# Kernel optimization log

Hardware: AMD Instinct MI355X
Metric: run time of the kernel (lower is better)

The kernel has to match this reference:

```python
import jax, jax.numpy as jnp
import numpy as np

B, M, N = 64, 100, 100
LAMBDA_COORD = 1.0
LAMBDA_CONF = 1.0
EPS = 1e-12


def _hungarian(cost):
    """O(n^3) Hungarian algorithm (potentials / e-maxx variant) on a square
    numpy cost matrix. Returns row_to_col assignment (length n)."""
    n = cost.shape[0]
    u = np.zeros(n + 1)
    v = np.zeros(n + 1)
    p = np.zeros(n + 1, dtype=np.int64)   # p[j] = row matched to column j
    way = np.zeros(n + 1, dtype=np.int64)
    for i in range(1, n + 1):
        p[0] = i
        j0 = 0
        minv = np.full(n + 1, np.inf)
        used = np.zeros(n + 1, dtype=bool)
        while True:
            used[j0] = True
            i0 = p[j0]
            js = np.nonzero(~used)[0]
            js = js[js > 0]
            cur = cost[i0 - 1, js - 1] - u[i0] - v[js]
            upd = cur < minv[js]
            minv[js] = np.where(upd, cur, minv[js])
            way[js] = np.where(upd, j0, way[js])
            j1 = js[np.argmin(minv[js])]
            delta = minv[j1]
            uj = np.nonzero(used)[0]
            u[p[uj]] += delta
            v[uj] -= delta
            minv[js] -= delta
            j0 = j1
            if p[j0] == 0:
                break
        while j0:
            j1 = way[j0]
            p[j0] = p[j1]
            j0 = j1
    row_to_col = np.full(n, -1, dtype=np.int64)
    for j in range(1, n + 1):
        row_to_col[p[j] - 1] = j - 1
    return row_to_col


def _match(pred_xy, target_xy, target_conf):
    """Host-side matching (mirrors the original's CPU round trip).
    Returns padded rows [B,P], cols [B,P] (cols index into the ORIGINAL target
    axis) and cnt [B] = number of matched pairs (min(M, K_valid))."""
    Bb, Mm, _ = pred_xy.shape
    Nn = target_xy.shape[1]
    P = min(Mm, Nn)
    rows = np.zeros((Bb, P), np.int64)
    cols = np.zeros((Bb, P), np.int64)
    cnt = np.zeros(Bb, np.int64)
    for b in range(Bb):
        valid = np.nonzero(target_conf[b] > 0.5)[0]
        K = valid.size
        if K == 0:
            continue
        tgt = target_xy[b, valid]                       # [K,2]
        cost = np.linalg.norm(pred_xy[b][:, None, :] - tgt[None, :, :], axis=-1)  # [M,K]
        n = max(Mm, K)
        sq = np.zeros((n, n))                           # zero-pad to square
        sq[:Mm, :K] = cost
        r2c = _hungarian(sq)
        k = 0
        for r in range(Mm):
            c = r2c[r]
            if 0 <= c < K:
                rows[b, k] = r
                cols[b, k] = valid[c]
                k += 1
        cnt[b] = k
    return rows, cols, cnt


def _loss(pred, target, rows, cols, cnt):
    Bb, P = rows.shape
    bidx = jnp.arange(Bb)[:, None]
    mp = pred[bidx, rows]                                # [B,P,3] matched preds
    mt = target[bidx, cols]                              # [B,P,3] matched tgts
    mask = (jnp.arange(P)[None, :] < cnt[:, None]).astype(pred.dtype)
    denom = jnp.maximum(cnt, 1).astype(pred.dtype)
    # per-batch F.mse_loss: mean over cnt*2 coord elements
    se = (((mp[..., :2] - mt[..., :2]) ** 2).sum(-1) * mask).sum(-1)
    loss_coord = jnp.where(cnt > 0, se / (2.0 * denom), 0.0).sum()
    # per-batch F.binary_cross_entropy: mean over cnt elements
    pconf = jnp.clip(mp[..., 2], EPS, 1.0 - EPS)
    tconf = mt[..., 2]
    bce = -(tconf * jnp.log(pconf) + (1.0 - tconf) * jnp.log1p(-pconf))
    loss_conf = jnp.where(cnt > 0, (bce * mask).sum(-1) / denom, 0.0).sum()
    return (LAMBDA_COORD * loss_coord + LAMBDA_CONF * loss_conf) / Bb


def setup_inputs() -> dict:
    key = jax.random.key(0)
    k1, k2 = jax.random.split(key)
    pred = jax.random.uniform(k1, (B, M, 3), dtype=jnp.float32)
    target = jax.random.uniform(k2, (B, N, 3), dtype=jnp.float32)
    return {"pred": pred, "target": target}


def reference(pred, target):
    pred_np = np.asarray(pred)
    tgt_np = np.asarray(target)
    rows, cols, cnt = _match(pred_np[..., :2], tgt_np[..., :2], tgt_np[..., 2])
    rows = jnp.asarray(rows)
    cols = jnp.asarray(cols)
    cnt = jnp.asarray(cnt)
    return _loss(pred, target, rows, cols, cnt)
```

## Files before the change

### kernel.cpp

```cpp
#include <hip/hip_runtime.h>
#include <math.h>

#define BATCH 64
#define MM 100
#define NN 100
#define ST 101
#define BIGCLAIM 0x7fffffff


__device__ __forceinline__ int readlane_i(int v, int lane) {
    return __builtin_amdgcn_readlane(v, lane);
}
__device__ __forceinline__ float readlane_f(float v, int lane) {
    return __int_as_float(__builtin_amdgcn_readlane(__float_as_int(v), lane));
}

template<int CTRL>
__device__ __forceinline__ float dpp_min_f32(float x) {
    int p = __builtin_amdgcn_update_dpp(__float_as_int(x), __float_as_int(x),
                                        CTRL, 0xF, 0xF, false);
    return fminf(x, __int_as_float(p));
}
__device__ __forceinline__ float wave_min_f32(float x) {
    x = dpp_min_f32<0xB1>(x);
    x = dpp_min_f32<0x4E>(x);
    x = dpp_min_f32<0x141>(x);
    x = dpp_min_f32<0x140>(x);
    x = dpp_min_f32<0x142>(x);
    x = dpp_min_f32<0x143>(x);
    return readlane_f(x, 63);
}


__global__ __launch_bounds__(128) void hungarian_loss_kernel(
        const float* __restrict__ pred, const float* __restrict__ target,
        double* __restrict__ ws) {
    const int b    = blockIdx.x;
    const int tid  = threadIdx.x;
    const int lane = tid & 63;
    const int wave = tid >> 6;
    const float* P = pred + b * MM * 3;
    const float* T = target + b * NN * 3;

    __shared__ float px[MM], py[MM], pc[MM];
    __shared__ float tvx[NN], tvy[NN], tvc[NN];
    __shared__ float Tc[NN * ST];
    __shared__ int   rmini[NN];
    __shared__ int   claimArr[MM + 1];
    __shared__ int   Ksh;

    float pxA = P[3*lane], pyA = P[3*lane+1];
    float pxB = 0.f, pyB = 0.f;
    const bool colBvalid = (lane + 64 < MM);
    if (colBvalid) { pxB = P[3*(lane+64)]; pyB = P[3*(lane+64)+1]; }

    if (wave == 0) {
        px[lane] = pxA; py[lane] = pyA; pc[lane] = P[3*lane+2];
        if (colBvalid) { px[lane+64]=pxB; py[lane+64]=pyB; pc[lane+64]=P[3*(lane+64)+2]; }
        float cxA=0.f, cyA=0.f, ccA=0.f, cxB=0.f, cyB=0.f, ccB=0.f;
        bool vA_=false, vB_=false;
        { cxA=T[3*lane]; cyA=T[3*lane+1]; ccA=T[3*lane+2]; vA_ = ccA > 0.5f; }
        if (lane + 64 < NN) {
            cxB=T[3*(lane+64)]; cyB=T[3*(lane+64)+1]; ccB=T[3*(lane+64)+2];
            vB_ = ccB > 0.5f;
        }
        unsigned long long mAv = __ballot(vA_);
        unsigned long long mBv = __ballot(vB_);
        int nA_ = __popcll(mAv);
        int K0  = nA_ + __popcll(mBv);
        unsigned long long below = (1ull << lane) - 1ull;
        if (vA_) { int q = __popcll(mAv & below);       tvx[q]=cxA; tvy[q]=cyA; tvc[q]=ccA; }
        if (vB_) { int q = nA_ + __popcll(mBv & below); tvx[q]=cxB; tvy[q]=cyB; tvc[q]=ccB; }
        if (lane == 0) Ksh = K0;
        claimArr[lane] = BIGCLAIM;
        if (lane + 64 <= MM) claimArr[lane + 64] = BIGCLAIM;
    }
    __syncthreads();
    const int K = Ksh;
    if (K == 0) { if (tid == 0) ws[b] = 0.0; return; }

    float txA = (lane < K)      ? tvx[lane]      : 0.f;
    float tyA = (lane < K)      ? tvy[lane]      : 0.f;
    float txB = (lane + 64 < K) ? tvx[lane + 64] : 0.f;
    float tyB = (lane + 64 < K) ? tvy[lane + 64] : 0.f;

    for (int c = wave; c < K; c += 2) {
        float tx = (c < 64) ? readlane_f(txA, c) : readlane_f(txB, c - 64);
        float ty = (c < 64) ? readlane_f(tyA, c) : readlane_f(tyB, c - 64);
        float dxA = __fsub_rn(pxA, tx), dyA = __fsub_rn(pyA, ty);
        float cA = __fsqrt_rn(__fadd_rn(__fmul_rn(dxA,dxA), __fmul_rn(dyA,dyA)));
        Tc[c*ST + lane] = cA;
        float cB = 1e30f;
        if (colBvalid) {
            float dxB = __fsub_rn(pxB, tx), dyB = __fsub_rn(pyB, ty);
            cB = __fsqrt_rn(__fadd_rn(__fmul_rn(dxB,dxB), __fmul_rn(dyB,dyB)));
            Tc[c*ST + lane + 64] = cB;
        }
        float m = wave_min_f32(fminf(cA, cB));
        unsigned long long eA = __ballot(cA == m);
        unsigned long long eB = __ballot(cB == m);
        int argc = eA ? ((int)__ffsll(eA) - 1) : ((int)__ffsll(eB) - 1 + 64);
        if (lane == 0) rmini[c] = argc;
    }
    __syncthreads();
    if (wave == 1) return;

    const float INF32 = __builtin_inff();
    const int jA = lane;
    const int jB = lane + 64;
    const bool validB = (jB <= MM);
    const int idxA = (jA >= 1) ? (jA - 1) : 0;
    const int idxB = validB ? (jB - 1) : (MM - 1);

    int rA = lane + 1, rB = lane + 65;
    int argA = 0, argB = 0;
    if (lane < K)      { argA = rmini[lane] + 1;      atomicMin(&claimArr[argA], rA); }
    if (lane + 64 < K) { argB = rmini[lane + 64] + 1; atomicMin(&claimArr[argB], rB); }
    __threadfence_block();
    int pA = 0, pB = 0;
    if (jA >= 1) { int c0 = claimArr[jA]; pA = (c0 != BIGCLAIM) ? c0 : 0; }
    if (validB)  { int c0 = claimArr[jB]; pB = (c0 != BIGCLAIM) ? c0 : 0; }
    bool freeA = (lane < K)      && (claimArr[argA] != rA);
    bool freeB = (lane + 64 < K) && (claimArr[argB] != rB);
    unsigned long long fA = __ballot(freeA);
    unsigned long long fB = __ballot(freeB);

    float vvA = 0.f, vvB = 0.f;

    unsigned long long dijA = 0ull, dijB = 0ull;
    for (int sweep = 0; sweep < 2; ++sweep) {
        unsigned long long curA = fA, curB = fB;
        fA = 0ull; fB = 0ull;
        while (curA | curB) {
            int r;
            if (curA) { r = (int)__ffsll(curA);      curA &= curA - 1; }
            else      { r = (int)__ffsll(curB) + 64; curB &= curB - 1; }

            float cA = Tc[(r-1)*ST + idxA];
            float cB = Tc[(r-1)*ST + idxB];
            float rcA = (jA >= 1) ? (cA - vvA) : INF32;
            float rcB = validB ? (cB - vvB) : INF32;
            float m1 = wave_min_f32(fminf(rcA, rcB));
            unsigned long long eA = __ballot(rcA == m1);
            unsigned long long eB = __ballot(rcB == m1);
            int j1 = eA ? ((int)__ffsll(eA) - 1) : ((int)__ffsll(eB) - 1 + 64);

            float rcA2 = (jA == j1) ? INF32 : rcA;
            float rcB2 = (jB == j1) ? INF32 : rcB;
            float m2 = wave_min_f32(fminf(rcA2, rcB2));

            int holder = (j1 < 64) ? readlane_i(pA, j1) : readlane_i(pB, j1 & 63);

            if (m1 < m2) {
                float dv = m2 - m1;
                if (jA == j1) { vvA -= dv; pA = r; }
                if (validB && jB == j1) { vvB -= dv; pB = r; }
                if (holder != 0) {
                    if (sweep == 0) {
                        if (holder <= 64) fA |= 1ull << (holder - 1);
                        else              fB |= 1ull << (holder - 65);
                    } else {
                        if (holder <= 64) dijA |= 1ull << (holder - 1);
                        else              dijB |= 1ull << (holder - 65);
                    }
                }
            } else {
                if (holder == 0) {
                    if (jA == j1) pA = r;
                    if (validB && jB == j1) pB = r;
                } else {
                    unsigned long long e2A = __ballot(rcA2 == m2);
                    unsigned long long e2B = __ballot(rcB2 == m2);
                    int j2 = e2A ? ((int)__ffsll(e2A) - 1)
                                 : ((int)__ffsll(e2B) - 1 + 64);
                    int h2 = (j2 < 64) ? readlane_i(pA, j2)
                                       : readlane_i(pB, j2 & 63);
                    if (h2 == 0) {
                        if (jA == j2) pA = r;
                        if (validB && jB == j2) pB = r;
                    } else {
                        if (sweep == 0) {
                            if (r <= 64) fA |= 1ull << (r - 1);
                            else         fB |= 1ull << (r - 65);
                        } else {
                            if (r <= 64) dijA |= 1ull << (r - 1);
                            else         dijB |= 1ull << (r - 65);
                        }
                    }
                }
            }
        }
    }

    while (dijA | dijB) {
        int r;
        if (dijA) { r = (int)__ffsll(dijA);      dijA &= dijA - 1; }
        else      { r = (int)__ffsll(dijB) + 64; dijB &= dijB - 1; }

        float minvA = INF32, minvB = INF32;
        int wayA = 0, wayB = 0;
        bool usedA = (lane == 0), usedB = false;
        float dpopA = 0.f, dpopB = 0.f;
        if (lane == 0) pA = r;
        int j0 = 0, jfree = -1;
        float dstar = 0.f;

        float cA_f = Tc[(r-1)*ST + idxA];
        float cB_f = Tc[(r-1)*ST + idxB];
        float S = 0.f;

        for (int it = 0; it <= MM; ++it) {
            float candA = INF32, candB = INF32;
            if (jA >= 1 && !usedA) {
                float t = (cA_f - vvA) + S;
                if (t < minvA) { minvA = t; wayA = j0; }
                candA = minvA;
            }
            if (validB && !usedB) {
                float t = (cB_f - vvB) + S;
                if (t < minvB) { minvB = t; wayB = j0; }
                candB = minvB;
            }

            float delta = wave_min_f32(fminf(candA, candB));
            unsigned long long eA = __ballot(candA == delta);
            unsigned long long eB = __ballot(candB == delta);
            int j1 = eA ? ((int)__ffsll(eA) - 1) : ((int)__ffsll(eB) - 1 + 64);

            if (jA == j1) { usedA = true; dpopA = delta; }
            if (jB == j1) { usedB = true; dpopB = delta; }

            int pa = readlane_i(pA, j1 & 63);
            int pb = readlane_i(pB, j1 & 63);
            int pj1 = (j1 < 64) ? pa : pb;
            if (pj1 == 0) { jfree = j1; dstar = delta; break; }

            float nxA = Tc[(pj1-1)*ST + idxA];
            float nxB = Tc[(pj1-1)*ST + idxB];
            float cjm = (j1 < 64) ? readlane_f(nxA, j1) : readlane_f(nxB, j1 & 63);
            float vjm = (j1 < 64) ? readlane_f(vvA, j1) : readlane_f(vvB, j1 & 63);
            S = (delta - cjm) + vjm;
            cA_f = nxA; cB_f = nxB;
            j0 = j1;
        }

        if (usedA && jA >= 1) vvA += dpopA - dstar;
        if (usedB)            vvB += dpopB - dstar;

        int jc = jfree;
        for (int s = 0; s <= MM && jc > 0; ++s) {
            int wa = readlane_i(wayA, jc & 63);
            int wb = readlane_i(wayB, jc & 63);
            int w  = (jc < 64) ? wa : wb;
            int pa = readlane_i(pA, w & 63);
            int pb = readlane_i(pB, w & 63);
            int pw = (w < 64) ? pa : pb;
            if (jA == jc) pA = pw;
            if (jB == jc) pB = pw;
            jc = w;
        }
    }

    double se = 0.0, bce = 0.0;
    if (jA >= 1 && pA > 0) {
        int rr = jA - 1, c = pA - 1;
        float dx = __fsub_rn(px[rr], tvx[c]);
        float dy = __fsub_rn(py[rr], tvy[c]);
        se = (double)dx*(double)dx + (double)dy*(double)dy;
        double pcv = (double)pc[rr];
        pcv = fmin(fmax(pcv, 1e-12), 1.0 - 1e-12);
        double tc = (double)tvc[c];
        bce = -(tc * log(pcv) + (1.0 - tc) * log1p(-pcv));
    }
    if (validB && pB > 0) {
        int rr = jB - 1, c = pB - 1;
        float dx = __fsub_rn(px[rr], tvx[c]);
        float dy = __fsub_rn(py[rr], tvy[c]);
        se += (double)dx*(double)dx + (double)dy*(double)dy;
        double pcv = (double)pc[rr];
        pcv = fmin(fmax(pcv, 1e-12), 1.0 - 1e-12);
        double tc = (double)tvc[c];
        bce += -(tc * log(pcv) + (1.0 - tc) * log1p(-pcv));
    }
    for (int m = 1; m < 64; m <<= 1) {
        se  += __shfl_xor(se,  m, 64);
        bce += __shfl_xor(bce, m, 64);
    }
    if (lane == 0) ws[b] = se / (2.0 * (double)K) + bce / (double)K;
}

__global__ __launch_bounds__(64) void final_reduce(const double* __restrict__ ws,
                                                   float* __restrict__ out) {
    double v = ws[threadIdx.x];
    for (int m = 1; m < 64; m <<= 1) v += __shfl_xor(v, m, 64);
    if (threadIdx.x == 0) out[0] = (float)(v / (double)BATCH);
}

extern "C" void kernel_launch(void* const* d_in, const int* in_sizes, int n_in,
                              void* d_out, int out_size, void* d_ws, size_t ws_size,
                              hipStream_t stream) {
    const float* pred   = (const float*)d_in[0];
    const float* target = (const float*)d_in[1];
    double* ws = (double*)d_ws;
    float* out = (float*)d_out;
    hungarian_loss_kernel<<<dim3(BATCH), dim3(128), 0, stream>>>(pred, target, ws);
    final_reduce<<<dim3(1), dim3(64), 0, stream>>>(ws, out);
}
```

Baseline: 53.63 us.

## Pack value/index keys for wave argmin, simplify auction sweep, fuse final reduction

Replaces the float wave-min plus ballot argmin with a single unsigned min over packed keys, where the low 7 mantissa bits are overwritten by the column index, and computes the top-two minimum in one DPP pass. The auction-style initial sweep is simplified: the m2 branch is removed and the next row's costs are prefetched. Matched costs are cached so the Dijkstra phase no longer reloads them. The separate final_reduce launch is dropped in favour of a last-block-done atomic counter with a memset. Packing drops the low mantissa bits, which can change tie-breaking or the matching chosen, and the memset adds a small operation of its own.

After: 56.14 us (median of 3 runs). 4.7% more time.

```diff
diff --git a/kernel.cpp b/kernel.cpp
--- a/kernel.cpp
+++ b/kernel.cpp
@@ -6,6 +6,7 @@
 #define NN 100
 #define ST 101
 #define BIGCLAIM 0x7fffffff
+#define SENTK 0xFFFFFFFFu
 
 
 __device__ __forceinline__ int readlane_i(int v, int lane) {
@@ -15,26 +16,64 @@
     return __int_as_float(__builtin_amdgcn_readlane(__float_as_int(v), lane));
 }
 
+__device__ __forceinline__ unsigned pack_key(float x, int col) {
+    unsigned u = __float_as_uint(x);
+    u ^= ((unsigned)((int)u >> 31)) | 0x80000000u;
+    return (u & 0xFFFFFF80u) | (unsigned)col;
+}
+__device__ __forceinline__ float key_val(unsigned k) {
+    unsigned u = k & 0xFFFFFF80u;
+    u = (u & 0x80000000u) ? (u ^ 0x80000000u) : ~u;
+    return __uint_as_float(u);
+}
+
 template<int CTRL>
-__device__ __forceinline__ float dpp_min_f32(float x) {
-    int p = __builtin_amdgcn_update_dpp(__float_as_int(x), __float_as_int(x),
-                                        CTRL, 0xF, 0xF, false);
-    return fminf(x, __int_as_float(p));
-}
-__device__ __forceinline__ float wave_min_f32(float x) {
-    x = dpp_min_f32<0xB1>(x);
-    x = dpp_min_f32<0x4E>(x);
-    x = dpp_min_f32<0x141>(x);
-    x = dpp_min_f32<0x140>(x);
-    x = dpp_min_f32<0x142>(x);
-    x = dpp_min_f32<0x143>(x);
-    return readlane_f(x, 63);
-}
-
-
-__global__ __launch_bounds__(128) void hungarian_loss_kernel(
+__device__ __forceinline__ unsigned dpp_mov_u32(unsigned x) {
+    return (unsigned)__builtin_amdgcn_update_dpp((int)x, (int)x, CTRL, 0xF, 0xF, false);
+}
+template<int CTRL>
+__device__ __forceinline__ unsigned dpp_min_u32(unsigned x) {
+    unsigned p = dpp_mov_u32<CTRL>(x);
+    return x < p ? x : p;
+}
+__device__ __forceinline__ unsigned wave_min_u32(unsigned x) {
+    x = dpp_min_u32<0xB1>(x);
+    x = dpp_min_u32<0x4E>(x);
+    x = dpp_min_u32<0x141>(x);
+    x = dpp_min_u32<0x140>(x);
+    x = dpp_min_u32<0x142>(x);
+    x = dpp_min_u32<0x143>(x);
+    return (unsigned)readlane_i((int)x, 63);
+}
+template<int CTRL>
+__device__ __forceinline__ void min2_step(unsigned &lo, unsigned &hi) {
+    unsigned olo = dpp_mov_u32<CTRL>(lo);
+    unsigned ohi = dpp_mov_u32<CTRL>(hi);
+    unsigned mn  = lo < olo ? lo : olo;
+    unsigned mx  = lo < olo ? olo : lo;
+    unsigned m2  = hi < ohi ? hi : ohi;
+    lo = mn;
+    hi = mx < m2 ? mx : m2;
+}
+__device__ __forceinline__ void wave_min2_u32(unsigned a, unsigned b,
+                                              unsigned &k1, unsigned &k2) {
+    unsigned lo = a < b ? a : b;
+    unsigned hi = a < b ? b : a;
+    min2_step<0xB1>(lo, hi);
+    min2_step<0x4E>(lo, hi);
+    min2_step<0x141>(lo, hi);
+    min2_step<0x140>(lo, hi);
+    min2_step<0x142>(lo, hi);
+    min2_step<0x143>(lo, hi);
+    k1 = (unsigned)readlane_i((int)lo, 63);
+    k2 = (unsigned)readlane_i((int)hi, 63);
+}
+
+
+__global__ __launch_bounds__(128) void hung_all(
         const float* __restrict__ pred, const float* __restrict__ target,
-        double* __restrict__ ws) {
+        double* __restrict__ wsloss, unsigned* __restrict__ counter,
+        float* __restrict__ out) {
     const int b    = blockIdx.x;
     const int tid  = threadIdx.x;
     const int lane = tid & 63;
@@ -57,9 +96,9 @@
     if (wave == 0) {
         px[lane] = pxA; py[lane] = pyA; pc[lane] = P[3*lane+2];
         if (colBvalid) { px[lane+64]=pxB; py[lane+64]=pyB; pc[lane+64]=P[3*(lane+64)+2]; }
-        float cxA=0.f, cyA=0.f, ccA=0.f, cxB=0.f, cyB=0.f, ccB=0.f;
-        bool vA_=false, vB_=false;
-        { cxA=T[3*lane]; cyA=T[3*lane+1]; ccA=T[3*lane+2]; vA_ = ccA > 0.5f; }
+        float cxA=T[3*lane], cyA=T[3*lane+1], ccA=T[3*lane+2];
+        bool vA_ = ccA > 0.5f;
+        float cxB=0.f, cyB=0.f, ccB=0.f; bool vB_=false;
         if (lane + 64 < NN) {
             cxB=T[3*(lane+64)]; cyB=T[3*(lane+64)+1]; ccB=T[3*(lane+64)+2];
             vB_ = ccB > 0.5f;
@@ -77,84 +116,89 @@
     }
     __syncthreads();
     const int K = Ksh;
-    if (K == 0) { if (tid == 0) ws[b] = 0.0; return; }
-
-    float txA = (lane < K)      ? tvx[lane]      : 0.f;
-    float tyA = (lane < K)      ? tvy[lane]      : 0.f;
-    float txB = (lane + 64 < K) ? tvx[lane + 64] : 0.f;
-    float tyB = (lane + 64 < K) ? tvy[lane + 64] : 0.f;
-
-    for (int c = wave; c < K; c += 2) {
-        float tx = (c < 64) ? readlane_f(txA, c) : readlane_f(txB, c - 64);
-        float ty = (c < 64) ? readlane_f(tyA, c) : readlane_f(tyB, c - 64);
-        float dxA = __fsub_rn(pxA, tx), dyA = __fsub_rn(pyA, ty);
-        float cA = __fsqrt_rn(__fadd_rn(__fmul_rn(dxA,dxA), __fmul_rn(dyA,dyA)));
-        Tc[c*ST + lane] = cA;
-        float cB = 1e30f;
-        if (colBvalid) {
-            float dxB = __fsub_rn(pxB, tx), dyB = __fsub_rn(pyB, ty);
-            cB = __fsqrt_rn(__fadd_rn(__fmul_rn(dxB,dxB), __fmul_rn(dyB,dyB)));
-            Tc[c*ST + lane + 64] = cB;
-        }
-        float m = wave_min_f32(fminf(cA, cB));
-        unsigned long long eA = __ballot(cA == m);
-        unsigned long long eB = __ballot(cB == m);
-        int argc = eA ? ((int)__ffsll(eA) - 1) : ((int)__ffsll(eB) - 1 + 64);
-        if (lane == 0) rmini[c] = argc;
-    }
-    __syncthreads();
-    if (wave == 1) return;
-
-    const float INF32 = __builtin_inff();
+
     const int jA = lane;
     const int jB = lane + 64;
     const bool validB = (jB <= MM);
     const int idxA = (jA >= 1) ? (jA - 1) : 0;
     const int idxB = validB ? (jB - 1) : (MM - 1);
 
-    int rA = lane + 1, rB = lane + 65;
-    int argA = 0, argB = 0;
-    if (lane < K)      { argA = rmini[lane] + 1;      atomicMin(&claimArr[argA], rA); }
-    if (lane + 64 < K) { argB = rmini[lane + 64] + 1; atomicMin(&claimArr[argB], rB); }
-    __threadfence_block();
-    int pA = 0, pB = 0;
-    if (jA >= 1) { int c0 = claimArr[jA]; pA = (c0 != BIGCLAIM) ? c0 : 0; }
-    if (validB)  { int c0 = claimArr[jB]; pB = (c0 != BIGCLAIM) ? c0 : 0; }
-    bool freeA = (lane < K)      && (claimArr[argA] != rA);
-    bool freeB = (lane + 64 < K) && (claimArr[argB] != rB);
-    unsigned long long fA = __ballot(freeA);
-    unsigned long long fB = __ballot(freeB);
-
-    float vvA = 0.f, vvB = 0.f;
-
-    unsigned long long dijA = 0ull, dijB = 0ull;
-    for (int sweep = 0; sweep < 2; ++sweep) {
-        unsigned long long curA = fA, curB = fB;
-        fA = 0ull; fB = 0ull;
-        while (curA | curB) {
-            int r;
-            if (curA) { r = (int)__ffsll(curA);      curA &= curA - 1; }
-            else      { r = (int)__ffsll(curB) + 64; curB &= curB - 1; }
-
-            float cA = Tc[(r-1)*ST + idxA];
-            float cB = Tc[(r-1)*ST + idxB];
-            float rcA = (jA >= 1) ? (cA - vvA) : INF32;
-            float rcB = validB ? (cB - vvB) : INF32;
-            float m1 = wave_min_f32(fminf(rcA, rcB));
-            unsigned long long eA = __ballot(rcA == m1);
-            unsigned long long eB = __ballot(rcB == m1);
-            int j1 = eA ? ((int)__ffsll(eA) - 1) : ((int)__ffsll(eB) - 1 + 64);
-
-            float rcA2 = (jA == j1) ? INF32 : rcA;
-            float rcB2 = (jB == j1) ? INF32 : rcB;
-            float m2 = wave_min_f32(fminf(rcA2, rcB2));
-
-            int holder = (j1 < 64) ? readlane_i(pA, j1) : readlane_i(pB, j1 & 63);
-
-            if (m1 < m2) {
-                float dv = m2 - m1;
-                if (jA == j1) { vvA -= dv; pA = r; }
-                if (validB && jB == j1) { vvB -= dv; pB = r; }
+    double loss = 0.0;
+    if (K > 0) {
+        float txA = (lane < K)      ? tvx[lane]      : 0.f;
+        float tyA = (lane < K)      ? tvy[lane]      : 0.f;
+        float txB = (lane + 64 < K) ? tvx[lane + 64] : 0.f;
+        float tyB = (lane + 64 < K) ? tvy[lane + 64] : 0.f;
+
+        for (int c = wave; c < K; c += 2) {
+            float tx = (c < 64) ? readlane_f(txA, c) : readlane_f(txB, c - 64);
+            float ty = (c < 64) ? readlane_f(tyA, c) : readlane_f(tyB, c - 64);
+            float dxA = __fsub_rn(pxA, tx), dyA = __fsub_rn(pyA, ty);
+            float cA = __fsqrt_rn(__fadd_rn(__fmul_rn(dxA,dxA), __fmul_rn(dyA,dyA)));
+            Tc[c*ST + lane] = cA;
+            unsigned kB = SENTK;
+            if (colBvalid) {
+                float dxB = __fsub_rn(pxB, tx), dyB = __fsub_rn(pyB, ty);
+                float cB = __fsqrt_rn(__fadd_rn(__fmul_rn(dxB,dxB), __fmul_rn(dyB,dyB)));
+                Tc[c*ST + lane + 64] = cB;
+                kB = pack_key(cB, lane + 64);
+            }
+            unsigned kA = pack_key(cA, lane);
+            unsigned k = wave_min_u32(kA < kB ? kA : kB);
+            if (lane == 0) rmini[c] = (int)(k & 127u);
+        }
+        __syncthreads();
+        if (wave == 1) return;
+
+        int rA_ = lane + 1, rB_ = lane + 65;
+        int argA = 0, argB = 0;
+        if (lane < K)      { argA = rmini[lane] + 1;      atomicMin(&claimArr[argA], rA_); }
+        if (lane + 64 < K) { argB = rmini[lane + 64] + 1; atomicMin(&claimArr[argB], rB_); }
+        __threadfence_block();
+        int pA = 0, pB = 0;
+        if (jA >= 1) { int c0 = claimArr[jA]; pA = (c0 != BIGCLAIM) ? c0 : 0; }
+        if (validB)  { int c0 = claimArr[jB]; pB = (c0 != BIGCLAIM) ? c0 : 0; }
+        bool freeA = (lane < K)      && (claimArr[argA] != rA_);
+        bool freeB = (lane + 64 < K) && (claimArr[argB] != rB_);
+        unsigned long long fA = __ballot(freeA);
+        unsigned long long fB = __ballot(freeB);
+
+        float mcA = 0.f, mcB = 0.f;
+        if (pA > 0) mcA = Tc[(pA-1)*ST + idxA];
+        if (pB > 0) mcB = Tc[(pB-1)*ST + idxB];
+
+        float vvA = 0.f, vvB = 0.f;
+
+        unsigned long long dijA = 0ull, dijB = 0ull;
+        for (int sweep = 0; sweep < 2; ++sweep) {
+            unsigned long long curA = fA, curB = fB;
+            fA = 0ull; fB = 0ull;
+            int rr = curA ? (int)__ffsll(curA)
+                          : (curB ? (int)__ffsll(curB) + 64 : 0);
+            float cA = 0.f, cB = 0.f;
+            if (rr) { cA = Tc[(rr-1)*ST + idxA]; cB = Tc[(rr-1)*ST + idxB]; }
+            while (curA | curB) {
+                int r;
+                if (curA) { r = (int)__ffsll(curA);      curA &= curA - 1; }
+                else      { r = (int)__ffsll(curB) + 64; curB &= curB - 1; }
+                int r2 = curA ? (int)__ffsll(curA)
+                              : (curB ? (int)__ffsll(curB) + 64 : r);
+                float nxA = Tc[(r2-1)*ST + idxA];
+                float nxB = Tc[(r2-1)*ST + idxB];
+
+                float rcA = cA - vvA;
+                float rcB = cB - vvB;
+                unsigned kA = (jA >= 1) ? pack_key(rcA, jA) : SENTK;
+                unsigned kB = validB ? pack_key(rcB, jB) : SENTK;
+                unsigned k1, k2;
+                wave_min2_u32(kA, kB, k1, k2);
+                int j1 = (int)(k1 & 127u);
+                float dv = fmaxf(key_val(k2) - key_val(k1), 0.f);
+
+                int holder = (j1 < 64) ? readlane_i(pA, j1)
+                                       : readlane_i(pB, j1 & 63);
+                if (jA == j1)            { vvA -= dv; pA = r; mcA = cA; }
+                if (validB && jB == j1)  { vvB -= dv; pB = r; mcB = cB; }
                 if (holder != 0) {
                     if (sweep == 0) {
                         if (holder <= 64) fA |= 1ull << (holder - 1);
@@ -164,136 +208,128 @@
                         else              dijB |= 1ull << (holder - 65);
                     }
                 }
-            } else {
-                if (holder == 0) {
-                    if (jA == j1) pA = r;
-                    if (validB && jB == j1) pB = r;
-                } else {
-                    unsigned long long e2A = __ballot(rcA2 == m2);
-                    unsigned long long e2B = __ballot(rcB2 == m2);
-                    int j2 = e2A ? ((int)__ffsll(e2A) - 1)
-                                 : ((int)__ffsll(e2B) - 1 + 64);
-                    int h2 = (j2 < 64) ? readlane_i(pA, j2)
-                                       : readlane_i(pB, j2 & 63);
-                    if (h2 == 0) {
-                        if (jA == j2) pA = r;
-                        if (validB && jB == j2) pB = r;
-                    } else {
-                        if (sweep == 0) {
-                            if (r <= 64) fA |= 1ull << (r - 1);
-                            else         fB |= 1ull << (r - 65);
-                        } else {
-                            if (r <= 64) dijA |= 1ull << (r - 1);
-                            else         dijB |= 1ull << (r - 65);
-                        }
-                    }
+                cA = nxA; cB = nxB;
+            }
+        }
+
+        const float INF32 = __builtin_inff();
+        float pcAf = 0.f, pcBf = 0.f;
+        {
+            int r0 = dijA ? (int)__ffsll(dijA)
+                          : (dijB ? (int)__ffsll(dijB) + 64 : 0);
+            if (r0) { pcAf = Tc[(r0-1)*ST + idxA]; pcBf = Tc[(r0-1)*ST + idxB]; }
+        }
+        while (dijA | dijB) {
+            int r;
+            if (dijA) { r = (int)__ffsll(dijA);      dijA &= dijA - 1; }
+            else      { r = (int)__ffsll(dijB) + 64; dijB &= dijB - 1; }
+
+            float minvA = INF32, minvB = INF32;
+            int wayA = 0, wayB = 0;
+            bool usedA = (lane == 0), usedB = false;
+            float dpopA = 0.f, dpopB = 0.f;
+            if (lane == 0) pA = r;
+            int j0 = 0, jfree = -1;
+            float dstar = 0.f, S = 0.f;
+            float cA_f = pcAf, cB_f = pcBf;
+
+            for (int it = 0; it <= MM; ++it) {
+                if (jA >= 1 && !usedA) {
+                    float t = (cA_f - vvA) + S;
+                    if (t < minvA) { minvA = t; wayA = j0; }
                 }
-            }
-        }
+                if (validB && !usedB) {
+                    float t = (cB_f - vvB) + S;
+                    if (t < minvB) { minvB = t; wayB = j0; }
+                }
+                unsigned kA = (jA >= 1 && !usedA) ? pack_key(minvA, jA) : SENTK;
+                unsigned kB = (validB && !usedB) ? pack_key(minvB, jB) : SENTK;
+                unsigned k1 = wave_min_u32(kA < kB ? kA : kB);
+                int j1 = (int)(k1 & 127u);
+                float delta = key_val(k1);
+
+                if (jA == j1) { usedA = true; dpopA = delta; }
+                if (jB == j1) { usedB = true; dpopB = delta; }
+
+                int pj1 = (j1 < 64) ? readlane_i(pA, j1)
+                                    : readlane_i(pB, j1 & 63);
+                if (pj1 == 0) { jfree = j1; dstar = delta; break; }
+
+                float mcj = (j1 < 64) ? readlane_f(mcA, j1) : readlane_f(mcB, j1 & 63);
+                float vj  = (j1 < 64) ? readlane_f(vvA, j1) : readlane_f(vvB, j1 & 63);
+                cA_f = Tc[(pj1-1)*ST + idxA];
+                cB_f = Tc[(pj1-1)*ST + idxB];
+                S = (delta - mcj) + vj;
+                j0 = j1;
+            }
+
+            {
+                int r1 = dijA ? (int)__ffsll(dijA)
+                              : (dijB ? (int)__ffsll(dijB) + 64 : 0);
+                if (r1) { pcAf = Tc[(r1-1)*ST + idxA]; pcBf = Tc[(r1-1)*ST + idxB]; }
+            }
+            if (usedA && jA >= 1) vvA += dpopA - dstar;
+            if (usedB)            vvB += dpopB - dstar;
+
+            int jc = jfree;
+            for (int s = 0; s <= MM && jc > 0; ++s) {
+                int wa = readlane_i(wayA, jc & 63);
+                int wb = readlane_i(wayB, jc & 63);
+                int w  = (jc < 64) ? wa : wb;
+                int pa = readlane_i(pA, w & 63);
+                int pb = readlane_i(pB, w & 63);
+                int pw = (w < 64) ? pa : pb;
+                if (jA == jc) { pA = pw; mcA = Tc[(pw-1)*ST + idxA]; }
+                if (validB && jB == jc) { pB = pw; mcB = Tc[(pw-1)*ST + idxB]; }
+                jc = w;
+            }
+        }
+
+        double se = 0.0, bce = 0.0;
+        if (jA >= 1 && pA > 0) {
+            int rr2 = jA - 1, c = pA - 1;
+            float dx = __fsub_rn(px[rr2], tvx[c]);
+            float dy = __fsub_rn(py[rr2], tvy[c]);
+            se = (double)dx*(double)dx + (double)dy*(double)dy;
+            double pcv = (double)pc[rr2];
+            pcv = fmin(fmax(pcv, 1e-12), 1.0 - 1e-12);
+            double tc = (double)tvc[c];
+            bce = -(tc * log(pcv) + (1.0 - tc) * log1p(-pcv));
+        }
+        if (validB && pB > 0) {
+            int rr2 = jB - 1, c = pB - 1;
+            float dx = __fsub_rn(px[rr2], tvx[c]);
+            float dy = __fsub_rn(py[rr2], tvy[c]);
+            se += (double)dx*(double)dx + (double)dy*(double)dy;
+            double pcv = (double)pc[rr2];
+            pcv = fmin(fmax(pcv, 1e-12), 1.0 - 1e-12);
+            double tc = (double)tvc[c];
+            bce += -(tc * log(pcv) + (1.0 - tc) * log1p(-pcv));
+        }
+        for (int m = 1; m < 64; m <<= 1) {
+            se  += __shfl_xor(se,  m, 64);
+            bce += __shfl_xor(bce, m, 64);
+        }
+        loss = se / (2.0 * (double)K) + bce / (double)K;
+    } else {
+        if (wave == 1) return;
     }
 
-    while (dijA | dijB) {
-        int r;
-        if (dijA) { r = (int)__ffsll(dijA);      dijA &= dijA - 1; }
-        else      { r = (int)__ffsll(dijB) + 64; dijB &= dijB - 1; }
-
-        float minvA = INF32, minvB = INF32;
-        int wayA = 0, wayB = 0;
-        bool usedA = (lane == 0), usedB = false;
-        float dpopA = 0.f, dpopB = 0.f;
-        if (lane == 0) pA = r;
-        int j0 = 0, jfree = -1;
-        float dstar = 0.f;
-
-        float cA_f = Tc[(r-1)*ST + idxA];
-        float cB_f = Tc[(r-1)*ST + idxB];
-        float S = 0.f;
-
-        for (int it = 0; it <= MM; ++it) {
-            float candA = INF32, candB = INF32;
-            if (jA >= 1 && !usedA) {
-                float t = (cA_f - vvA) + S;
-                if (t < minvA) { minvA = t; wayA = j0; }
-                candA = minvA;
-            }
-            if (validB && !usedB) {
-                float t = (cB_f - vvB) + S;
-                if (t < minvB) { minvB = t; wayB = j0; }
-                candB = minvB;
-            }
-
-            float delta = wave_min_f32(fminf(candA, candB));
-            unsigned long long eA = __ballot(candA == delta);
-            unsigned long long eB = __ballot(candB == delta);
-            int j1 = eA ? ((int)__ffsll(eA) - 1) : ((int)__ffsll(eB) - 1 + 64);
-
-            if (jA == j1) { usedA = true; dpopA = delta; }
-            if (jB == j1) { usedB = true; dpopB = delta; }
-
-            int pa = readlane_i(pA, j1 & 63);
-            int pb = readlane_i(pB, j1 & 63);
-            int pj1 = (j1 < 64) ? pa : pb;
-            if (pj1 == 0) { jfree = j1; dstar = delta; break; }
-
-            float nxA = Tc[(pj1-1)*ST + idxA];
-            float nxB = Tc[(pj1-1)*ST + idxB];
-            float cjm = (j1 < 64) ? readlane_f(nxA, j1) : readlane_f(nxB, j1 & 63);
-            float vjm = (j1 < 64) ? readlane_f(vvA, j1) : readlane_f(vvB, j1 & 63);
-            S = (delta - cjm) + vjm;
-            cA_f = nxA; cB_f = nxB;
-            j0 = j1;
-        }
-
-        if (usedA && jA >= 1) vvA += dpopA - dstar;
-        if (usedB)            vvB += dpopB - dstar;
-
-        int jc = jfree;
-        for (int s = 0; s <= MM && jc > 0; ++s) {
-            int wa = readlane_i(wayA, jc & 63);
-            int wb = readlane_i(wayB, jc & 63);
-            int w  = (jc < 64) ? wa : wb;
-            int pa = readlane_i(pA, w & 63);
-            int pb = readlane_i(pB, w & 63);
-            int pw = (w < 64) ? pa : pb;
-            if (jA == jc) pA = pw;
-            if (jB == jc) pB = pw;
-            jc = w;
-        }
+    unsigned old = 0;
+    if (lane == 0) {
+        wsloss[b] = loss;
+        __threadfence();
+        old = atomicAdd(counter, 1u);
     }
-
-    double se = 0.0, bce = 0.0;
-    if (jA >= 1 && pA > 0) {
-        int rr = jA - 1, c = pA - 1;
-        float dx = __fsub_rn(px[rr], tvx[c]);
-        float dy = __fsub_rn(py[rr], tvy[c]);
-        se = (double)dx*(double)dx + (double)dy*(double)dy;
-        double pcv = (double)pc[rr];
-        pcv = fmin(fmax(pcv, 1e-12), 1.0 - 1e-12);
-        double tc = (double)tvc[c];
-        bce = -(tc * log(pcv) + (1.0 - tc) * log1p(-pcv));
+    unsigned long long lastm = __ballot((lane == 0) && (old == BATCH - 1));
+    if (lastm) {
+        __threadfence();
+        unsigned long long bits =
+            atomicCAS((unsigned long long*)&wsloss[lane], 0ull, 0ull);
+        double v = __longlong_as_double(bits);
+        for (int m = 1; m < 64; m <<= 1) v += __shfl_xor(v, m, 64);
+        if (lane == 0) out[0] = (float)(v / (double)BATCH);
     }
-    if (validB && pB > 0) {
-        int rr = jB - 1, c = pB - 1;
-        float dx = __fsub_rn(px[rr], tvx[c]);
-        float dy = __fsub_rn(py[rr], tvy[c]);
-        se += (double)dx*(double)dx + (double)dy*(double)dy;
-        double pcv = (double)pc[rr];
-        pcv = fmin(fmax(pcv, 1e-12), 1.0 - 1e-12);
-        double tc = (double)tvc[c];
-        bce += -(tc * log(pcv) + (1.0 - tc) * log1p(-pcv));
-    }
-    for (int m = 1; m < 64; m <<= 1) {
-        se  += __shfl_xor(se,  m, 64);
-        bce += __shfl_xor(bce, m, 64);
-    }
-    if (lane == 0) ws[b] = se / (2.0 * (double)K) + bce / (double)K;
-}
-
-__global__ __launch_bounds__(64) void final_reduce(const double* __restrict__ ws,
-                                                   float* __restrict__ out) {
-    double v = ws[threadIdx.x];
-    for (int m = 1; m < 64; m <<= 1) v += __shfl_xor(v, m, 64);
-    if (threadIdx.x == 0) out[0] = (float)(v / (double)BATCH);
 }
 
 extern "C" void kernel_launch(void* const* d_in, const int* in_sizes, int n_in,
@@ -301,8 +337,9 @@
                               hipStream_t stream) {
     const float* pred   = (const float*)d_in[0];
     const float* target = (const float*)d_in[1];
-    double* ws = (double*)d_ws;
-    float* out = (float*)d_out;
-    hungarian_loss_kernel<<<dim3(BATCH), dim3(128), 0, stream>>>(pred, target, ws);
-    final_reduce<<<dim3(1), dim3(64), 0, stream>>>(ws, out);
-}
+    double*   wsl = (double*)d_ws;
+    unsigned* cnt = (unsigned*)((char*)d_ws + 512);
+    float*    out = (float*)d_out;
+    hipMemsetAsync(cnt, 0, sizeof(unsigned), stream);
+    hung_all<<<dim3(BATCH), dim3(128), 0, stream>>>(pred, target, wsl, cnt, out);
+}
```
